# Kernel optimization log

Measured on AMD Instinct MI355X. Metric: run time of the kernel, lower is better.

The kernel has to match this reference:

```python
import jax, jax.numpy as jnp
import numpy as np
from jax import lax

IN_CH = 512
OUT_CH = 512
HEAD_DIM = 8
NUM_HEADS = IN_CH // HEAD_DIM  # 64
INNER = NUM_HEADS * HEAD_DIM   # 512
KSIZE = 5
EPS = 1e-15
BN_EPS = 1e-5
DN = ('NCHW', 'OIHW', 'NCHW')


def setup_inputs() -> dict:
    key = jax.random.key(0)
    ks = jax.random.split(key, 10)
    s = 0.02
    return {
        'hidden_states': jax.random.normal(ks[0], (4, IN_CH, 64, 64), jnp.float32),
        'wq': jax.random.normal(ks[1], (INNER, IN_CH), jnp.float32) * s,
        'wk': jax.random.normal(ks[2], (INNER, IN_CH), jnp.float32) * s,
        'wv': jax.random.normal(ks[3], (INNER, IN_CH), jnp.float32) * s,
        # depthwise conv: groups = 3*INNER, 1 in-channel per group
        'dw_kernel': jax.random.normal(ks[4], (3 * INNER, 1, KSIZE, KSIZE), jnp.float32) * s,
        # grouped 1x1 conv: groups = 3*NUM_HEADS -> 3*INNER/(3*NUM_HEADS)=HEAD_DIM in-ch/group
        'pw_kernel': jax.random.normal(ks[5], (3 * INNER, HEAD_DIM, 1, 1), jnp.float32) * s,
        # proj_out 1x1: in = INNER*(1+len(kernel_sizes)) = 2*INNER
        'proj_kernel': jax.random.normal(ks[6], (OUT_CH, 2 * INNER, 1, 1), jnp.float32) * s,
        'bn_gamma': jnp.ones((OUT_CH,), jnp.float32),
        'bn_beta': jnp.zeros((OUT_CH,), jnp.float32),
        'bn_mean': jnp.zeros((OUT_CH,), jnp.float32),
        'bn_var': jnp.ones((OUT_CH,), jnp.float32),
    }


def _forward(hidden_states, wq, wk, wv, dw_kernel, pw_kernel, proj_kernel,
             bn_gamma, bn_beta, bn_mean, bn_var):
    x = hidden_states  # [B,C,H,W]
    B, _, H, W = x.shape
    h = jnp.moveaxis(x, 1, -1)  # [B,H,W,C]
    q = h @ wq.T
    k = h @ wk.T
    v = h @ wv.T
    qkv = jnp.moveaxis(jnp.concatenate([q, k, v], axis=-1), -1, 1)  # [B,3*INNER,H,W]

    # multi-scale aggregation: depthwise 5x5 then grouped 1x1
    dw = lax.conv_general_dilated(qkv, dw_kernel, (1, 1), 'SAME',
                                  feature_group_count=3 * INNER, dimension_numbers=DN)
    pw = lax.conv_general_dilated(dw, pw_kernel, (1, 1), 'VALID',
                                  feature_group_count=3 * NUM_HEADS, dimension_numbers=DN)
    qkv_all = jnp.concatenate([qkv, pw], axis=1)  # [B, 2*3*INNER, H, W]

    # relu linear attention (fp32)
    N = H * W
    d = HEAD_DIM
    f = qkv_all.astype(jnp.float32).reshape(B, -1, 3 * d, N)  # [B, nh_total, 3d, N]
    query = jax.nn.relu(f[:, :, :d])
    key_ = jax.nn.relu(f[:, :, d:2 * d])
    value = f[:, :, 2 * d:]
    value_pad = jnp.concatenate([value, jnp.ones_like(value[:, :, :1])], axis=2)  # [B,nh,d+1,N]
    scores = jnp.einsum('bhdn,bhen->bhde', value_pad, key_)   # [B,nh,d+1,d]
    out = jnp.einsum('bhde,bhen->bhdn', scores, query)         # [B,nh,d+1,N]
    out = out[:, :, :-1] / (out[:, :, -1:] + EPS)
    out = out.reshape(B, -1, H, W).astype(qkv_all.dtype)        # [B, 2*INNER, H, W]

    # proj_out 1x1 conv + BatchNorm2d (eval mode, running stats)
    y = lax.conv_general_dilated(out, proj_kernel, (1, 1), 'VALID', dimension_numbers=DN)
    inv = bn_gamma / jnp.sqrt(bn_var + BN_EPS)
    y = y * inv[None, :, None, None] + (bn_beta - bn_mean * inv)[None, :, None, None]
    return y + x


def reference(hidden_states, wq, wk, wv, dw_kernel, pw_kernel, proj_kernel,
              bn_gamma, bn_beta, bn_mean, bn_var):
    return _forward(hidden_states, wq, wk, wv, dw_kernel, pw_kernel, proj_kernel,
                    bn_gamma, bn_beta, bn_mean, bn_var)
```

## Files before the change

### kernel.cpp

```cpp
#include <hip/hip_runtime.h>
#include <hip/hip_bf16.h>

typedef __hip_bfloat16 bf16;
typedef __attribute__((ext_vector_type(8))) short bf16x8;
typedef __attribute__((ext_vector_type(4))) float f32x4;

#define BATCH 4
#define CIN   512
#define HW    64
#define NPIX  4096
#define CALL  3072
#define NHEAD 128
#define EPS_LITE 1e-15f
#define BN_EPS   1e-5f


__device__ __forceinline__ short f2bf(float f) {
    __hip_bfloat16 h = __float2bfloat16(f);
    short s; __builtin_memcpy(&s, &h, 2); return s;
}
__device__ __forceinline__ float bfl(unsigned u) {
    unsigned v = u << 16; float f; __builtin_memcpy(&f, &v, 4); return f;
}
__device__ __forceinline__ float bfh(unsigned u) {
    unsigned v = u & 0xffff0000u; float f; __builtin_memcpy(&f, &v, 4); return f;
}
__device__ __forceinline__ unsigned packbf(float a, float b) {
    return (unsigned)(unsigned short)f2bf(a) | ((unsigned)(unsigned short)f2bf(b) << 16);
}
__device__ __forceinline__ void gll16(const void* gsrc, void* ldst) {
    __builtin_amdgcn_global_load_lds(
        (const __attribute__((address_space(1))) unsigned int*)gsrc,
        (__attribute__((address_space(3))) unsigned int*)ldst, 16, 0, 0);
}

__global__ __launch_bounds__(256) void k_cvtw(const float* __restrict__ wq,
                                              const float* __restrict__ wk,
                                              const float* __restrict__ wv,
                                              const float* __restrict__ pj,
                                              bf16* __restrict__ Wbf,
                                              bf16* __restrict__ Pbf) {
    const int e = (blockIdx.x * 256 + threadIdx.x) * 4;
    const float* s; bf16* dst;
    if (e < 786432) {
        int o;
        if (e < 262144)      { s = wq; o = e; }
        else if (e < 524288) { s = wk; o = e - 262144; }
        else                 { s = wv; o = e - 524288; }
        f32x4 v = *(const f32x4*)(s + o);
        dst = Wbf + e;
        *(ushort2*)dst = make_ushort2((unsigned short)f2bf(v[0]), (unsigned short)f2bf(v[1]));
        *(ushort2*)(dst + 2) = make_ushort2((unsigned short)f2bf(v[2]), (unsigned short)f2bf(v[3]));
    } else {
        const int o = e - 786432;
        f32x4 v = *(const f32x4*)(pj + o);
        dst = Pbf + o;
        *(ushort2*)dst = make_ushort2((unsigned short)f2bf(v[0]), (unsigned short)f2bf(v[1]));
        *(ushort2*)(dst + 2) = make_ushort2((unsigned short)f2bf(v[2]), (unsigned short)f2bf(v[3]));
    }
}

__global__ __launch_bounds__(256) void k_cvtx(const float* __restrict__ x,
                                              bf16* __restrict__ xT) {
    __shared__ short lds[64][72];
    const int t   = threadIdx.x;
    const int px0 = blockIdx.x * 64;
    const int k0  = blockIdx.y * 64;
    const int b   = blockIdx.z;

    const int pr = t & 15, rr = t >> 4;
#pragma unroll
    for (int it = 0; it < 4; ++it) {
        const int row = it * 16 + rr;
        f32x4 v = *(const f32x4*)(x + (size_t)(b * CIN + k0 + row) * NPIX + px0 + pr * 4);
#pragma unroll
        for (int i = 0; i < 4; ++i) lds[pr * 4 + i][row] = f2bf(v[i]);
    }
    __syncthreads();

    const int px = t >> 2, kc = t & 3;
    uint4 u0 = *(const uint4*)&lds[px][kc * 16];
    uint4 u1 = *(const uint4*)&lds[px][kc * 16 + 8];
    bf16* dst = xT + ((size_t)b * NPIX + px0 + px) * 512 + k0 + kc * 16;
    *(uint4*)dst = u0;
    *(uint4*)(dst + 8) = u1;
}

template<int KD, int MT, bool PROJ>
__global__ __launch_bounds__(256) void k_gemm3(
        const bf16* __restrict__ Xt,
        const bf16* __restrict__ Wb,
        bf16* __restrict__ Obf,
        const float* __restrict__ gm, const float* __restrict__ bt,
        const float* __restrict__ mu, const float* __restrict__ va,
        const float* __restrict__ resid, float* __restrict__ Of)
{
    constexpr int NT = KD / 32;
    constexpr int MS = MT / 32;
    constexpr int AG = MT / 64;
    __shared__ short Ald[2][MT * 32];
    __shared__ short Bld[2][128 * 32];

    const int t    = threadIdx.x;
    const int lane = t & 63;
    const int w    = t >> 6;
    const int wm   = w >> 1, wn = w & 1;
    const int n0   = blockIdx.x * 128;
    const int c0   = blockIdx.y * MT;
    const int b    = blockIdx.z;

    const bf16* abase = Wb + (size_t)(c0 + w * (MT / 4) + (lane >> 2)) * KD + (lane & 3) * 8;
    const bf16* bbase = Xt + ((size_t)b * NPIX + n0 + w * 32 + (lane >> 2)) * KD + (lane & 3) * 8;

    auto stage = [&](int s, int buf) {
#pragma unroll
        for (int q = 0; q < AG; ++q)
            gll16(abase + (size_t)q * 16 * KD + s * 32,
                  &Ald[buf][(w * (MT / 4) + q * 16) * 32]);
#pragma unroll
        for (int q = 0; q < 2; ++q)
            gll16(bbase + (size_t)q * 16 * KD + s * 32,
                  &Bld[buf][(w * 32 + q * 16) * 32]);
    };

    f32x4 acc[MS][4];
#pragma unroll
    for (int ms = 0; ms < MS; ++ms)
#pragma unroll
        for (int ns = 0; ns < 4; ++ns)
#pragma unroll
            for (int j = 0; j < 4; ++j) acc[ms][ns][j] = 0.f;

    stage(0, 0);
    __syncthreads();

    const int l15 = lane & 15, l4 = lane >> 4;
    for (int s = 0; s < NT; ++s) {
        const int cur = s & 1;
        if (s + 1 < NT) stage(s + 1, cur ^ 1);

        bf16x8 af[MS], bv[4];
#pragma unroll
        for (int ms = 0; ms < MS; ++ms)
            af[ms] = *(const bf16x8*)&Ald[cur][(wm * (MT / 2) + ms * 16 + l15) * 32 + l4 * 8];
#pragma unroll
        for (int ns = 0; ns < 4; ++ns)
            bv[ns] = *(const bf16x8*)&Bld[cur][(wn * 64 + ns * 16 + l15) * 32 + l4 * 8];
#pragma unroll
        for (int ms = 0; ms < MS; ++ms)
#pragma unroll
            for (int ns = 0; ns < 4; ++ns)
                acc[ms][ns] = __builtin_amdgcn_mfma_f32_16x16x32_bf16(
                    af[ms], bv[ns], acc[ms][ns], 0, 0, 0);

        __syncthreads();
    }

    if (!PROJ) {
#pragma unroll
        for (int ms = 0; ms < MS; ++ms) {
            const int crow = c0 + wm * (MT / 2) + ms * 16 + l4 * 4;
#pragma unroll
            for (int ns = 0; ns < 4; ++ns) {
                const int ncol = n0 + wn * 64 + ns * 16 + l15;
#pragma unroll
                for (int j = 0; j < 4; ++j) {
                    bf16 h; short sv = f2bf(acc[ms][ns][j]);
                    __builtin_memcpy(&h, &sv, 2);
                    Obf[((size_t)b * CALL + crow + j) * NPIX + ncol] = h;
                }
            }
        }
    } else {
#pragma unroll
        for (int ms = 0; ms < MS; ++ms) {
            const int crow = c0 + wm * (MT / 2) + ms * 16 + l4 * 4;
#pragma unroll
            for (int j = 0; j < 4; ++j) {
                const int o = crow + j;
                const float inv = gm[o] / sqrtf(va[o] + BN_EPS);
                const float sh  = bt[o] - mu[o] * inv;
#pragma unroll
                for (int ns = 0; ns < 4; ++ns) {
                    const int ncol = n0 + wn * 64 + ns * 16 + l15;
                    const size_t idx = ((size_t)b * 512 + o) * NPIX + ncol;
                    Of[idx] = acc[ms][ns][j] * inv + sh + resid[idx];
                }
            }
        }
    }
}

#define DW_ICS 1608
#define DW_DCS 1032
__global__ __launch_bounds__(256) void k_dwpw(const float* __restrict__ dwk,
                                              const float* __restrict__ pwk,
                                              bf16* __restrict__ qkv_all) {
    __shared__ short slds[8 * DW_ICS];

    const int t  = threadIdx.x;
    const int g  = blockIdx.y;
    const int b  = blockIdx.z;
    const int y0 = blockIdx.x * 16;

    const bf16* src = qkv_all + ((size_t)b * CALL + g * 8) * NPIX;
#pragma unroll
    for (int i = 0; i < 7; ++i) {
        const int v = i * 256 + t;
        if (v < 1600) {
            const int ch  = v / 200;
            const int rem = v % 200;
            const int row = rem / 10;
            const int seg = rem % 10;
            const int grow = y0 + row - 2;
            uint4 val = make_uint4(0u, 0u, 0u, 0u);
            if (seg >= 1 && seg <= 8 && grow >= 0 && grow < HW)
                val = *(const uint4*)(src + (size_t)ch * NPIX + grow * HW + (seg - 1) * 8);
            *(uint4*)&slds[ch * DW_ICS + row * 80 + seg * 8] = val;
        }
    }

    const int lane = t & 63;
    const int w    = t >> 6;
    const int xb   = lane & 7;
    const int ch   = lane >> 3;
    const int x0   = xb * 8;

    float kc[25];
    {
        const float* kp = dwk + (size_t)(g * 8 + ch) * 25;
#pragma unroll
        for (int i = 0; i < 25; ++i) kc[i] = kp[i];
    }
    __syncthreads();

    float A[5][12];
    const short* cb = &slds[ch * DW_ICS + x0];

    auto loadrow = [&](int L, float* f) {
        const short* rp = cb + L * 80;
        uint2 lo = *(const uint2*)(rp + 4);
        uint4 md = *(const uint4*)(rp + 8);
        uint2 hi = *(const uint2*)(rp + 16);
        f[0]  = bfl(lo.y); f[1]  = bfh(lo.y);
        f[2]  = bfl(md.x); f[3]  = bfh(md.x);
        f[4]  = bfl(md.y); f[5]  = bfh(md.y);
        f[6]  = bfl(md.z); f[7]  = bfh(md.z);
        f[8]  = bfl(md.w); f[9]  = bfh(md.w);
        f[10] = bfl(hi.x); f[11] = bfh(hi.x);
    };

    const int r0 = w * 4;
    loadrow(r0 + 0, A[0]);
    loadrow(r0 + 1, A[1]);
    loadrow(r0 + 2, A[2]);
    loadrow(r0 + 3, A[3]);

    uint4 pk[4];
#pragma unroll
    for (int ri = 0; ri < 4; ++ri) {
        loadrow(r0 + ri + 4, A[(ri + 4) % 5]);
        float acc[8];
#pragma unroll
        for (int i = 0; i < 8; ++i) acc[i] = 0.f;
#pragma unroll
        for (int dy = 0; dy < 5; ++dy) {
            const float* Ar = A[(ri + dy) % 5];
#pragma unroll
            for (int dx = 0; dx < 5; ++dx) {
                const float kv = kc[dy * 5 + dx];
#pragma unroll
                for (int i = 0; i < 8; ++i)
                    acc[i] += Ar[i + dx] * kv;
            }
        }
        pk[ri].x = packbf(acc[0], acc[1]);
        pk[ri].y = packbf(acc[2], acc[3]);
        pk[ri].z = packbf(acc[4], acc[5]);
        pk[ri].w = packbf(acc[6], acc[7]);
    }
    __syncthreads();

#pragma unroll
    for (int ri = 0; ri < 4; ++ri)
        *(uint4*)&slds[ch * DW_DCS + (r0 + ri) * 64 + x0] = pk[ri];
    __syncthreads();

    const float* pwb = pwk + (size_t)g * 64;
#pragma unroll
    for (int it = 0; it < 2; ++it) {
        const int p2 = (it * 256 + t) * 2;
        float v0[8], v1[8];
#pragma unroll
        for (int ci = 0; ci < 8; ++ci) {
            const unsigned u = *(const unsigned*)&slds[ci * DW_DCS + p2];
            v0[ci] = bfl(u); v1[ci] = bfh(u);
        }
        bf16* op = qkv_all + ((size_t)b * CALL + 1536 + g * 8) * NPIX + y0 * HW + p2;
#pragma unroll
        for (int o = 0; o < 8; ++o) {
            float s0 = 0.f, s1 = 0.f;
#pragma unroll
            for (int ci = 0; ci < 8; ++ci) {
                const float wv = pwb[o * 8 + ci];
                s0 += wv * v0[ci]; s1 += wv * v1[ci];
            }
            *(unsigned*)(op + (size_t)o * NPIX) = packbf(s0, s1);
        }
    }
}

__global__ __launch_bounds__(64) void k_scores(const bf16* __restrict__ qkv_all,
                                               float* __restrict__ part) {
    const int lane = threadIdx.x;
    const int h = blockIdx.y;
    const int b = blockIdx.z;
    const bf16* base = qkv_all + ((size_t)b * CALL + h * 24) * NPIX;

    float acc[72];
#pragma unroll
    for (int i = 0; i < 72; ++i) acc[i] = 0.f;

    for (int it = 0; it < 4; ++it) {
        const int n = blockIdx.x * 512 + it * 128 + lane * 2;
        const bf16* p = base + n;
        float k0[8], k1[8], v0[8], v1[8];
#pragma unroll
        for (int e = 0; e < 8; ++e) {
            const unsigned u = *(const unsigned*)&p[(size_t)(8 + e) * NPIX];
            k0[e] = fmaxf(bfl(u), 0.f); k1[e] = fmaxf(bfh(u), 0.f);
        }
#pragma unroll
        for (int d = 0; d < 8; ++d) {
            const unsigned u = *(const unsigned*)&p[(size_t)(16 + d) * NPIX];
            v0[d] = bfl(u); v1[d] = bfh(u);
        }
#pragma unroll
        for (int d = 0; d < 9; ++d) {
            const float vd0 = (d < 8) ? v0[d] : 1.f;
            const float vd1 = (d < 8) ? v1[d] : 1.f;
#pragma unroll
            for (int e = 0; e < 8; ++e)
                acc[d * 8 + e] += vd0 * k0[e] + vd1 * k1[e];
        }
    }

    const int bh = b * NHEAD + h;
#pragma unroll
    for (int i = 0; i < 72; ++i) {
        float v = acc[i];
        for (int off = 32; off; off >>= 1) v += __shfl_xor(v, off, 64);
        if (lane == 0) part[((size_t)bh * 72 + i) * 8 + blockIdx.x] = v;
    }
}

__global__ __launch_bounds__(256) void k_att3(const bf16* __restrict__ qkv_all,
                                              const float* __restrict__ part,
                                              bf16* __restrict__ attT) {
    __shared__ float sc[72];
    const int t  = threadIdx.x;
    const int h  = blockIdx.y;
    const int b  = blockIdx.z;
    const int bh = b * NHEAD + h;

    if (t < 72) {
        float s = 0.f;
#pragma unroll
        for (int ns = 0; ns < 8; ++ns) s += part[((size_t)bh * 72 + t) * 8 + ns];
        sc[t] = s;
    }
    __syncthreads();

    const int px = blockIdx.x * 256 + t;
    const bf16* qb = qkv_all + ((size_t)b * CALL + h * 24) * NPIX + px;
    float q[8];
#pragma unroll
    for (int e = 0; e < 8; ++e)
        q[e] = fmaxf(__bfloat162float(qb[(size_t)e * NPIX]), 0.f);

    float num[9];
#pragma unroll
    for (int d = 0; d < 9; ++d) {
        float s = 0.f;
#pragma unroll
        for (int e = 0; e < 8; ++e) s += sc[d * 8 + e] * q[e];
        num[d] = s;
    }
    const float inv = 1.f / (num[8] + EPS_LITE);
    uint4 pk;
    pk.x = packbf(num[0] * inv, num[1] * inv);
    pk.y = packbf(num[2] * inv, num[3] * inv);
    pk.z = packbf(num[4] * inv, num[5] * inv);
    pk.w = packbf(num[6] * inv, num[7] * inv);
    *(uint4*)(attT + ((size_t)b * NPIX + px) * 1024 + h * 8) = pk;
}

extern "C" void kernel_launch(void* const* d_in, const int* in_sizes, int n_in,
                              void* d_out, int out_size, void* d_ws, size_t ws_size,
                              hipStream_t stream) {
    const float* x   = (const float*)d_in[0];
    const float* wq  = (const float*)d_in[1];
    const float* wk  = (const float*)d_in[2];
    const float* wv  = (const float*)d_in[3];
    const float* dwk = (const float*)d_in[4];
    const float* pwk = (const float*)d_in[5];
    const float* pj  = (const float*)d_in[6];
    const float* gm  = (const float*)d_in[7];
    const float* bt  = (const float*)d_in[8];
    const float* mu  = (const float*)d_in[9];
    const float* va  = (const float*)d_in[10];
    float* out = (float*)d_out;

    char* ws = (char*)d_ws;
    bf16*  qkv_all = (bf16*)(ws);
    bf16*  attT    = (bf16*)(ws + 100663296);
    bf16*  xT      = (bf16*)(ws + 100663296);
    float* part    = (float*)(ws + 134217728);
    bf16*  Wbf     = (bf16*)(ws + 135544832);
    bf16*  Pbf     = (bf16*)(ws + 137117696);

    k_cvtw<<<dim3(1280), 256, 0, stream>>>(wq, wk, wv, pj, Wbf, Pbf);
    k_cvtx<<<dim3(64, 8, BATCH), 256, 0, stream>>>(x, xT);
    k_gemm3<512, 128, false><<<dim3(32, 12, BATCH), 256, 0, stream>>>(
        xT, Wbf, qkv_all, nullptr, nullptr, nullptr, nullptr, nullptr, nullptr);
    k_dwpw  <<<dim3( 4, 192, BATCH), 256, 0, stream>>>(dwk, pwk, qkv_all);
    k_scores<<<dim3( 8, 128, BATCH),  64, 0, stream>>>(qkv_all, part);
    k_att3  <<<dim3(16, 128, BATCH), 256, 0, stream>>>(qkv_all, part, attT);
    k_gemm3<1024, 64, true><<<dim3(32, 8, BATCH), 256, 0, stream>>>(
        attT, Pbf, nullptr, gm, bt, mu, va, x, out);
}
```

Baseline: 172.9 us.

## Merge conversion kernels and co-schedule independent attention stages in shared launches

Merges the weight and input conversion kernels into one launch. The depthwise/pointwise stage now shares a launch with the scores computation for the first 64 heads, which depend only on the GEMM output. A second launch pairs scores for the upper heads with attention output for the lower heads, and the remaining attention runs in a third launch. The aim is fewer launches and better GPU fill by overlapping independent work, at the cost of extra branching and shared-memory sizing set by the largest body.

New measurement: 226.0 us. +30.8%, slower.

```diff
diff --git a/kernel.cpp b/kernel.cpp
--- a/kernel.cpp
+++ b/kernel.cpp
@@ -34,56 +34,59 @@
         (__attribute__((address_space(3))) unsigned int*)ldst, 16, 0, 0);
 }
 
-__global__ __launch_bounds__(256) void k_cvtw(const float* __restrict__ wq,
-                                              const float* __restrict__ wk,
-                                              const float* __restrict__ wv,
-                                              const float* __restrict__ pj,
-                                              bf16* __restrict__ Wbf,
-                                              bf16* __restrict__ Pbf) {
-    const int e = (blockIdx.x * 256 + threadIdx.x) * 4;
-    const float* s; bf16* dst;
-    if (e < 786432) {
-        int o;
-        if (e < 262144)      { s = wq; o = e; }
-        else if (e < 524288) { s = wk; o = e - 262144; }
-        else                 { s = wv; o = e - 524288; }
-        f32x4 v = *(const f32x4*)(s + o);
-        dst = Wbf + e;
-        *(ushort2*)dst = make_ushort2((unsigned short)f2bf(v[0]), (unsigned short)f2bf(v[1]));
-        *(ushort2*)(dst + 2) = make_ushort2((unsigned short)f2bf(v[2]), (unsigned short)f2bf(v[3]));
+__global__ __launch_bounds__(256) void k_cvt(const float* __restrict__ x,
+                                             const float* __restrict__ wq,
+                                             const float* __restrict__ wk,
+                                             const float* __restrict__ wv,
+                                             const float* __restrict__ pj,
+                                             bf16* __restrict__ xT,
+                                             bf16* __restrict__ Wbf,
+                                             bf16* __restrict__ Pbf) {
+    __shared__ short lds[64][72];
+    const int bid = blockIdx.x;
+    const int t   = threadIdx.x;
+
+    if (bid < 2048) {
+        const int px0 = (bid & 63) * 64;
+        const int k0  = ((bid >> 6) & 7) * 64;
+        const int b   = bid >> 9;
+
+        const int pr = t & 15, rr = t >> 4;
+#pragma unroll
+        for (int it = 0; it < 4; ++it) {
+            const int row = it * 16 + rr;
+            f32x4 v = *(const f32x4*)(x + (size_t)(b * CIN + k0 + row) * NPIX + px0 + pr * 4);
+#pragma unroll
+            for (int i = 0; i < 4; ++i) lds[pr * 4 + i][row] = f2bf(v[i]);
+        }
+        __syncthreads();
+
+        const int px = t >> 2, kc = t & 3;
+        uint4 u0 = *(const uint4*)&lds[px][kc * 16];
+        uint4 u1 = *(const uint4*)&lds[px][kc * 16 + 8];
+        bf16* dst = xT + ((size_t)b * NPIX + px0 + px) * 512 + k0 + kc * 16;
+        *(uint4*)dst = u0;
+        *(uint4*)(dst + 8) = u1;
     } else {
-        const int o = e - 786432;
-        f32x4 v = *(const f32x4*)(pj + o);
-        dst = Pbf + o;
-        *(ushort2*)dst = make_ushort2((unsigned short)f2bf(v[0]), (unsigned short)f2bf(v[1]));
-        *(ushort2*)(dst + 2) = make_ushort2((unsigned short)f2bf(v[2]), (unsigned short)f2bf(v[3]));
-    }
-}
-
-__global__ __launch_bounds__(256) void k_cvtx(const float* __restrict__ x,
-                                              bf16* __restrict__ xT) {
-    __shared__ short lds[64][72];
-    const int t   = threadIdx.x;
-    const int px0 = blockIdx.x * 64;
-    const int k0  = blockIdx.y * 64;
-    const int b   = blockIdx.z;
-
-    const int pr = t & 15, rr = t >> 4;
-#pragma unroll
-    for (int it = 0; it < 4; ++it) {
-        const int row = it * 16 + rr;
-        f32x4 v = *(const f32x4*)(x + (size_t)(b * CIN + k0 + row) * NPIX + px0 + pr * 4);
-#pragma unroll
-        for (int i = 0; i < 4; ++i) lds[pr * 4 + i][row] = f2bf(v[i]);
-    }
-    __syncthreads();
-
-    const int px = t >> 2, kc = t & 3;
-    uint4 u0 = *(const uint4*)&lds[px][kc * 16];
-    uint4 u1 = *(const uint4*)&lds[px][kc * 16 + 8];
-    bf16* dst = xT + ((size_t)b * NPIX + px0 + px) * 512 + k0 + kc * 16;
-    *(uint4*)dst = u0;
-    *(uint4*)(dst + 8) = u1;
+        const int e = ((bid - 2048) * 256 + t) * 4;
+        const float* s; bf16* dst;
+        if (e < 786432) {
+            int o;
+            if (e < 262144)      { s = wq; o = e; }
+            else if (e < 524288) { s = wk; o = e - 262144; }
+            else                 { s = wv; o = e - 524288; }
+            f32x4 v = *(const f32x4*)(s + o);
+            dst = Wbf + e;
+            *(ushort2*)dst = make_ushort2((unsigned short)f2bf(v[0]), (unsigned short)f2bf(v[1]));
+            *(ushort2*)(dst + 2) = make_ushort2((unsigned short)f2bf(v[2]), (unsigned short)f2bf(v[3]));
+        } else {
+            const int o = e - 786432;
+            f32x4 v = *(const f32x4*)(pj + o);
+            dst = Pbf + o;
+            *(ushort2*)dst = make_ushort2((unsigned short)f2bf(v[0]), (unsigned short)f2bf(v[1]));
+            *(ushort2*)(dst + 2) = make_ushort2((unsigned short)f2bf(v[2]), (unsigned short)f2bf(v[3]));
+        }
+    }
 }
 
 template<int KD, int MT, bool PROJ>
@@ -193,15 +196,14 @@
 
 #define DW_ICS 1608
 #define DW_DCS 1032
-__global__ __launch_bounds__(256) void k_dwpw(const float* __restrict__ dwk,
-                                              const float* __restrict__ pwk,
-                                              bf16* __restrict__ qkv_all) {
-    __shared__ short slds[8 * DW_ICS];
-
+
+__device__ __forceinline__ void dwpw_body(const float* __restrict__ dwk,
+                                          const float* __restrict__ pwk,
+                                          bf16* __restrict__ qkv_all,
+                                          short* slds,
+                                          int ytile, int g, int b) {
     const int t  = threadIdx.x;
-    const int g  = blockIdx.y;
-    const int b  = blockIdx.z;
-    const int y0 = blockIdx.x * 16;
+    const int y0 = ytile * 16;
 
     const bf16* src = qkv_all + ((size_t)b * CALL + g * 8) * NPIX;
 #pragma unroll
@@ -310,11 +312,10 @@
     }
 }
 
-__global__ __launch_bounds__(64) void k_scores(const bf16* __restrict__ qkv_all,
-                                               float* __restrict__ part) {
-    const int lane = threadIdx.x;
-    const int h = blockIdx.y;
-    const int b = blockIdx.z;
+__device__ __forceinline__ void scores_body(const bf16* __restrict__ qkv_all,
+                                            float* __restrict__ part,
+                                            int ns, int h, int b) {
+    const int lane = threadIdx.x & 63;
     const bf16* base = qkv_all + ((size_t)b * CALL + h * 24) * NPIX;
 
     float acc[72];
@@ -322,7 +323,7 @@
     for (int i = 0; i < 72; ++i) acc[i] = 0.f;
 
     for (int it = 0; it < 4; ++it) {
-        const int n = blockIdx.x * 512 + it * 128 + lane * 2;
+        const int n = ns * 512 + it * 128 + lane * 2;
         const bf16* p = base + n;
         float k0[8], k1[8], v0[8], v1[8];
 #pragma unroll
@@ -350,28 +351,27 @@
     for (int i = 0; i < 72; ++i) {
         float v = acc[i];
         for (int off = 32; off; off >>= 1) v += __shfl_xor(v, off, 64);
-        if (lane == 0) part[((size_t)bh * 72 + i) * 8 + blockIdx.x] = v;
-    }
-}
-
-__global__ __launch_bounds__(256) void k_att3(const bf16* __restrict__ qkv_all,
-                                              const float* __restrict__ part,
-                                              bf16* __restrict__ attT) {
-    __shared__ float sc[72];
+        if (lane == 0) part[((size_t)bh * 72 + i) * 8 + ns] = v;
+    }
+}
+
+__device__ __forceinline__ void att_body(const bf16* __restrict__ qkv_all,
+                                         const float* __restrict__ part,
+                                         bf16* __restrict__ attT,
+                                         float* sc,
+                                         int xt, int h, int b) {
     const int t  = threadIdx.x;
-    const int h  = blockIdx.y;
-    const int b  = blockIdx.z;
     const int bh = b * NHEAD + h;
 
     if (t < 72) {
         float s = 0.f;
 #pragma unroll
-        for (int ns = 0; ns < 8; ++ns) s += part[((size_t)bh * 72 + t) * 8 + ns];
+        for (int nss = 0; nss < 8; ++nss) s += part[((size_t)bh * 72 + t) * 8 + nss];
         sc[t] = s;
     }
     __syncthreads();
 
-    const int px = blockIdx.x * 256 + t;
+    const int px = xt * 256 + t;
     const bf16* qb = qkv_all + ((size_t)b * CALL + h * 24) * NPIX + px;
     float q[8];
 #pragma unroll
@@ -393,6 +393,46 @@
     pk.z = packbf(num[4] * inv, num[5] * inv);
     pk.w = packbf(num[6] * inv, num[7] * inv);
     *(uint4*)(attT + ((size_t)b * NPIX + px) * 1024 + h * 8) = pk;
+}
+
+__global__ __launch_bounds__(256, 4) void k_fuse1(const float* __restrict__ dwk,
+                                                  const float* __restrict__ pwk,
+                                                  bf16* __restrict__ qkv_all,
+                                                  float* __restrict__ part) {
+    __shared__ short slds[8 * DW_ICS];
+    const int bid = blockIdx.x;
+    if (bid < 512) {
+        const int ns = bid & 7, hg = (bid >> 3) & 15, b = bid >> 7;
+        const int h  = hg * 4 + (threadIdx.x >> 6);
+        scores_body(qkv_all, part, ns, h, b);
+    } else {
+        const int db = bid - 512;
+        const int ytile = db & 3, g = (db >> 2) % 192, b = db / 768;
+        dwpw_body(dwk, pwk, qkv_all, slds, ytile, g, b);
+    }
+}
+
+__global__ __launch_bounds__(256, 4) void k_fuse2(const bf16* __restrict__ qkv_all,
+                                                  float* __restrict__ part,
+                                                  bf16* __restrict__ attT) {
+    __shared__ float sc[72];
+    const int bid = blockIdx.x;
+    if (bid < 512) {
+        const int ns = bid & 7, hg = (bid >> 3) & 15, b = bid >> 7;
+        const int h  = 64 + hg * 4 + (threadIdx.x >> 6);
+        scores_body(qkv_all, part, ns, h, b);
+    } else {
+        const int ab = bid - 512;
+        const int xt = ab & 15, h = (ab >> 4) & 63, b = ab >> 10;
+        att_body(qkv_all, part, attT, sc, xt, h, b);
+    }
+}
+
+__global__ __launch_bounds__(256) void k_att_hi(const bf16* __restrict__ qkv_all,
+                                                const float* __restrict__ part,
+                                                bf16* __restrict__ attT) {
+    __shared__ float sc[72];
+    att_body(qkv_all, part, attT, sc, blockIdx.x, blockIdx.y + 64, blockIdx.z);
 }
 
 extern "C" void kernel_launch(void* const* d_in, const int* in_sizes, int n_in,
@@ -419,13 +459,12 @@
     bf16*  Wbf     = (bf16*)(ws + 135544832);
     bf16*  Pbf     = (bf16*)(ws + 137117696);
 
-    k_cvtw<<<dim3(1280), 256, 0, stream>>>(wq, wk, wv, pj, Wbf, Pbf);
-    k_cvtx<<<dim3(64, 8, BATCH), 256, 0, stream>>>(x, xT);
+    k_cvt<<<dim3(3328), 256, 0, stream>>>(x, wq, wk, wv, pj, xT, Wbf, Pbf);
     k_gemm3<512, 128, false><<<dim3(32, 12, BATCH), 256, 0, stream>>>(
         xT, Wbf, qkv_all, nullptr, nullptr, nullptr, nullptr, nullptr, nullptr);
-    k_dwpw  <<<dim3( 4, 192, BATCH), 256, 0, stream>>>(dwk, pwk, qkv_all);
-    k_scores<<<dim3( 8, 128, BATCH),  64, 0, stream>>>(qkv_all, part);
-    k_att3  <<<dim3(16, 128, BATCH), 256, 0, stream>>>(qkv_all, part, attT);
+    k_fuse1 <<<dim3(3584), 256, 0, stream>>>(dwk, pwk, qkv_all, part);
+    k_fuse2 <<<dim3(4608), 256, 0, stream>>>(qkv_all, part, attT);
+    k_att_hi<<<dim3(16, 64, BATCH), 256, 0, stream>>>(qkv_all, part, attT);
     k_gemm3<1024, 64, true><<<dim3(32, 8, BATCH), 256, 0, stream>>>(
         attT, Pbf, nullptr, gm, bt, mu, va, x, out);
 }
```

## Merge conversion kernels and double-buffer row tiles in depthwise/pointwise kernel

Applied to the files above, without the earlier changes.

The weight and input conversion kernels are combined into one launch that picks its role from the block index, removing one kernel launch. The depthwise+pointwise kernel now handles two 16-row tiles per block and prefetches the second tile's global loads into registers while the first tile is computed, to hide load latency. The pointwise accumulation is written as 2-wide float vector operations. In exchange it uses more registers, which may lower occupancy, and launches half as many dwpw blocks.

Result: faster. 166.8 us (-3.5%).

```diff
diff --git a/kernel.cpp b/kernel.cpp
--- a/kernel.cpp
+++ b/kernel.cpp
@@ -4,6 +4,7 @@
 typedef __hip_bfloat16 bf16;
 typedef __attribute__((ext_vector_type(8))) short bf16x8;
 typedef __attribute__((ext_vector_type(4))) float f32x4;
+typedef __attribute__((ext_vector_type(2))) float f32v2;
 
 #define BATCH 4
 #define CIN   512
@@ -34,56 +35,59 @@
         (__attribute__((address_space(3))) unsigned int*)ldst, 16, 0, 0);
 }
 
-__global__ __launch_bounds__(256) void k_cvtw(const float* __restrict__ wq,
-                                              const float* __restrict__ wk,
-                                              const float* __restrict__ wv,
-                                              const float* __restrict__ pj,
-                                              bf16* __restrict__ Wbf,
-                                              bf16* __restrict__ Pbf) {
-    const int e = (blockIdx.x * 256 + threadIdx.x) * 4;
-    const float* s; bf16* dst;
-    if (e < 786432) {
-        int o;
-        if (e < 262144)      { s = wq; o = e; }
-        else if (e < 524288) { s = wk; o = e - 262144; }
-        else                 { s = wv; o = e - 524288; }
-        f32x4 v = *(const f32x4*)(s + o);
-        dst = Wbf + e;
-        *(ushort2*)dst = make_ushort2((unsigned short)f2bf(v[0]), (unsigned short)f2bf(v[1]));
-        *(ushort2*)(dst + 2) = make_ushort2((unsigned short)f2bf(v[2]), (unsigned short)f2bf(v[3]));
+__global__ __launch_bounds__(256) void k_cvt(const float* __restrict__ x,
+                                             const float* __restrict__ wq,
+                                             const float* __restrict__ wk,
+                                             const float* __restrict__ wv,
+                                             const float* __restrict__ pj,
+                                             bf16* __restrict__ xT,
+                                             bf16* __restrict__ Wbf,
+                                             bf16* __restrict__ Pbf) {
+    __shared__ short lds[64][72];
+    const int bid = blockIdx.x;
+    const int t   = threadIdx.x;
+
+    if (bid < 2048) {
+        const int px0 = (bid & 63) * 64;
+        const int k0  = ((bid >> 6) & 7) * 64;
+        const int b   = bid >> 9;
+
+        const int pr = t & 15, rr = t >> 4;
+#pragma unroll
+        for (int it = 0; it < 4; ++it) {
+            const int row = it * 16 + rr;
+            f32x4 v = *(const f32x4*)(x + (size_t)(b * CIN + k0 + row) * NPIX + px0 + pr * 4);
+#pragma unroll
+            for (int i = 0; i < 4; ++i) lds[pr * 4 + i][row] = f2bf(v[i]);
+        }
+        __syncthreads();
+
+        const int px = t >> 2, kc = t & 3;
+        uint4 u0 = *(const uint4*)&lds[px][kc * 16];
+        uint4 u1 = *(const uint4*)&lds[px][kc * 16 + 8];
+        bf16* dst = xT + ((size_t)b * NPIX + px0 + px) * 512 + k0 + kc * 16;
+        *(uint4*)dst = u0;
+        *(uint4*)(dst + 8) = u1;
     } else {
-        const int o = e - 786432;
-        f32x4 v = *(const f32x4*)(pj + o);
-        dst = Pbf + o;
-        *(ushort2*)dst = make_ushort2((unsigned short)f2bf(v[0]), (unsigned short)f2bf(v[1]));
-        *(ushort2*)(dst + 2) = make_ushort2((unsigned short)f2bf(v[2]), (unsigned short)f2bf(v[3]));
-    }
-}
-
-__global__ __launch_bounds__(256) void k_cvtx(const float* __restrict__ x,
-                                              bf16* __restrict__ xT) {
-    __shared__ short lds[64][72];
-    const int t   = threadIdx.x;
-    const int px0 = blockIdx.x * 64;
-    const int k0  = blockIdx.y * 64;
-    const int b   = blockIdx.z;
-
-    const int pr = t & 15, rr = t >> 4;
-#pragma unroll
-    for (int it = 0; it < 4; ++it) {
-        const int row = it * 16 + rr;
-        f32x4 v = *(const f32x4*)(x + (size_t)(b * CIN + k0 + row) * NPIX + px0 + pr * 4);
-#pragma unroll
-        for (int i = 0; i < 4; ++i) lds[pr * 4 + i][row] = f2bf(v[i]);
-    }
-    __syncthreads();
-
-    const int px = t >> 2, kc = t & 3;
-    uint4 u0 = *(const uint4*)&lds[px][kc * 16];
-    uint4 u1 = *(const uint4*)&lds[px][kc * 16 + 8];
-    bf16* dst = xT + ((size_t)b * NPIX + px0 + px) * 512 + k0 + kc * 16;
-    *(uint4*)dst = u0;
-    *(uint4*)(dst + 8) = u1;
+        const int e = ((bid - 2048) * 256 + t) * 4;
+        const float* s; bf16* dst;
+        if (e < 786432) {
+            int o;
+            if (e < 262144)      { s = wq; o = e; }
+            else if (e < 524288) { s = wk; o = e - 262144; }
+            else                 { s = wv; o = e - 524288; }
+            f32x4 v = *(const f32x4*)(s + o);
+            dst = Wbf + e;
+            *(ushort2*)dst = make_ushort2((unsigned short)f2bf(v[0]), (unsigned short)f2bf(v[1]));
+            *(ushort2*)(dst + 2) = make_ushort2((unsigned short)f2bf(v[2]), (unsigned short)f2bf(v[3]));
+        } else {
+            const int o = e - 786432;
+            f32x4 v = *(const f32x4*)(pj + o);
+            dst = Pbf + o;
+            *(ushort2*)dst = make_ushort2((unsigned short)f2bf(v[0]), (unsigned short)f2bf(v[1]));
+            *(ushort2*)(dst + 2) = make_ushort2((unsigned short)f2bf(v[2]), (unsigned short)f2bf(v[3]));
+        }
+    }
 }
 
 template<int KD, int MT, bool PROJ>
@@ -198,27 +202,12 @@
                                               bf16* __restrict__ qkv_all) {
     __shared__ short slds[8 * DW_ICS];
 
-    const int t  = threadIdx.x;
-    const int g  = blockIdx.y;
-    const int b  = blockIdx.z;
-    const int y0 = blockIdx.x * 16;
+    const int t   = threadIdx.x;
+    const int g   = blockIdx.y;
+    const int b   = blockIdx.z;
+    const int yt0 = blockIdx.x * 2;
 
     const bf16* src = qkv_all + ((size_t)b * CALL + g * 8) * NPIX;
-#pragma unroll
-    for (int i = 0; i < 7; ++i) {
-        const int v = i * 256 + t;
-        if (v < 1600) {
-            const int ch  = v / 200;
-            const int rem = v % 200;
-            const int row = rem / 10;
-            const int seg = rem % 10;
-            const int grow = y0 + row - 2;
-            uint4 val = make_uint4(0u, 0u, 0u, 0u);
-            if (seg >= 1 && seg <= 8 && grow >= 0 && grow < HW)
-                val = *(const uint4*)(src + (size_t)ch * NPIX + grow * HW + (seg - 1) * 8);
-            *(uint4*)&slds[ch * DW_ICS + row * 80 + seg * 8] = val;
-        }
-    }
 
     const int lane = t & 63;
     const int w    = t >> 6;
@@ -226,88 +215,132 @@
     const int ch   = lane >> 3;
     const int x0   = xb * 8;
 
+    const int sv   = t;
+    auto tload = [&](int ytile, uint4* r) {
+        const int y0 = ytile * 16;
+#pragma unroll
+        for (int i = 0; i < 7; ++i) {
+            const int v = i * 256 + sv;
+            uint4 val = make_uint4(0u, 0u, 0u, 0u);
+            if (v < 1600) {
+                const int c  = v / 200;
+                const int rm = v % 200;
+                const int rw = rm / 10;
+                const int sg = rm % 10;
+                const int grow = y0 + rw - 2;
+                if (sg >= 1 && sg <= 8 && grow >= 0 && grow < HW)
+                    val = *(const uint4*)(src + (size_t)c * NPIX + grow * HW + (sg - 1) * 8);
+            }
+            r[i] = val;
+        }
+    };
+    auto twrite = [&](const uint4* r) {
+#pragma unroll
+        for (int i = 0; i < 7; ++i) {
+            const int v = i * 256 + sv;
+            if (v < 1600) {
+                const int c  = v / 200;
+                const int rm = v % 200;
+                const int rw = rm / 10;
+                const int sg = rm % 10;
+                *(uint4*)&slds[c * DW_ICS + rw * 80 + sg * 8] = r[i];
+            }
+        }
+    };
+
     float kc[25];
     {
         const float* kp = dwk + (size_t)(g * 8 + ch) * 25;
 #pragma unroll
         for (int i = 0; i < 25; ++i) kc[i] = kp[i];
     }
+
+    auto compute_tile = [&](int ytile) {
+        const int y0 = ytile * 16;
+        float A[5][12];
+        const short* cb = &slds[ch * DW_ICS + x0];
+
+        auto loadrow = [&](int L, float* f) {
+            const short* rp = cb + L * 80;
+            uint2 lo = *(const uint2*)(rp + 4);
+            uint4 md = *(const uint4*)(rp + 8);
+            uint2 hi = *(const uint2*)(rp + 16);
+            f[0]  = bfl(lo.y); f[1]  = bfh(lo.y);
+            f[2]  = bfl(md.x); f[3]  = bfh(md.x);
+            f[4]  = bfl(md.y); f[5]  = bfh(md.y);
+            f[6]  = bfl(md.z); f[7]  = bfh(md.z);
+            f[8]  = bfl(md.w); f[9]  = bfh(md.w);
+            f[10] = bfl(hi.x); f[11] = bfh(hi.x);
+        };
+
+        const int rr0 = w * 4;
+        loadrow(rr0 + 0, A[0]);
+        loadrow(rr0 + 1, A[1]);
+        loadrow(rr0 + 2, A[2]);
+        loadrow(rr0 + 3, A[3]);
+
+        uint4 pk[4];
+#pragma unroll
+        for (int ri = 0; ri < 4; ++ri) {
+            loadrow(rr0 + ri + 4, A[(ri + 4) % 5]);
+            float acc[8];
+#pragma unroll
+            for (int i = 0; i < 8; ++i) acc[i] = 0.f;
+#pragma unroll
+            for (int dy = 0; dy < 5; ++dy) {
+                const float* Ar = A[(ri + dy) % 5];
+#pragma unroll
+                for (int dx = 0; dx < 5; ++dx) {
+                    const float kv = kc[dy * 5 + dx];
+#pragma unroll
+                    for (int i = 0; i < 8; ++i)
+                        acc[i] += Ar[i + dx] * kv;
+                }
+            }
+            pk[ri].x = packbf(acc[0], acc[1]);
+            pk[ri].y = packbf(acc[2], acc[3]);
+            pk[ri].z = packbf(acc[4], acc[5]);
+            pk[ri].w = packbf(acc[6], acc[7]);
+        }
+        __syncthreads();
+
+#pragma unroll
+        for (int ri = 0; ri < 4; ++ri)
+            *(uint4*)&slds[ch * DW_DCS + (rr0 + ri) * 64 + x0] = pk[ri];
+        __syncthreads();
+
+        const float* pwb = pwk + (size_t)g * 64;
+#pragma unroll
+        for (int it2 = 0; it2 < 2; ++it2) {
+            const int p2 = (it2 * 256 + t) * 2;
+            f32v2 v2[8];
+#pragma unroll
+            for (int ci = 0; ci < 8; ++ci) {
+                const unsigned u = *(const unsigned*)&slds[ci * DW_DCS + p2];
+                v2[ci][0] = bfl(u); v2[ci][1] = bfh(u);
+            }
+            bf16* op = qkv_all + ((size_t)b * CALL + 1536 + g * 8) * NPIX + y0 * HW + p2;
+#pragma unroll
+            for (int o = 0; o < 8; ++o) {
+                f32v2 s2 = {0.f, 0.f};
+#pragma unroll
+                for (int ci = 0; ci < 8; ++ci)
+                    s2 += pwb[o * 8 + ci] * v2[ci];
+                *(unsigned*)(op + (size_t)o * NPIX) = packbf(s2[0], s2[1]);
+            }
+        }
+    };
+
+    uint4 rA[7], rB[7];
+    tload(yt0, rA);
+    twrite(rA);
     __syncthreads();
-
-    float A[5][12];
-    const short* cb = &slds[ch * DW_ICS + x0];
-
-    auto loadrow = [&](int L, float* f) {
-        const short* rp = cb + L * 80;
-        uint2 lo = *(const uint2*)(rp + 4);
-        uint4 md = *(const uint4*)(rp + 8);
-        uint2 hi = *(const uint2*)(rp + 16);
-        f[0]  = bfl(lo.y); f[1]  = bfh(lo.y);
-        f[2]  = bfl(md.x); f[3]  = bfh(md.x);
-        f[4]  = bfl(md.y); f[5]  = bfh(md.y);
-        f[6]  = bfl(md.z); f[7]  = bfh(md.z);
-        f[8]  = bfl(md.w); f[9]  = bfh(md.w);
-        f[10] = bfl(hi.x); f[11] = bfh(hi.x);
-    };
-
-    const int r0 = w * 4;
-    loadrow(r0 + 0, A[0]);
-    loadrow(r0 + 1, A[1]);
-    loadrow(r0 + 2, A[2]);
-    loadrow(r0 + 3, A[3]);
-
-    uint4 pk[4];
-#pragma unroll
-    for (int ri = 0; ri < 4; ++ri) {
-        loadrow(r0 + ri + 4, A[(ri + 4) % 5]);
-        float acc[8];
-#pragma unroll
-        for (int i = 0; i < 8; ++i) acc[i] = 0.f;
-#pragma unroll
-        for (int dy = 0; dy < 5; ++dy) {
-            const float* Ar = A[(ri + dy) % 5];
-#pragma unroll
-            for (int dx = 0; dx < 5; ++dx) {
-                const float kv = kc[dy * 5 + dx];
-#pragma unroll
-                for (int i = 0; i < 8; ++i)
-                    acc[i] += Ar[i + dx] * kv;
-            }
-        }
-        pk[ri].x = packbf(acc[0], acc[1]);
-        pk[ri].y = packbf(acc[2], acc[3]);
-        pk[ri].z = packbf(acc[4], acc[5]);
-        pk[ri].w = packbf(acc[6], acc[7]);
-    }
+    tload(yt0 + 1, rB);
+    compute_tile(yt0);
     __syncthreads();
-
-#pragma unroll
-    for (int ri = 0; ri < 4; ++ri)
-        *(uint4*)&slds[ch * DW_DCS + (r0 + ri) * 64 + x0] = pk[ri];
+    twrite(rB);
     __syncthreads();
-
-    const float* pwb = pwk + (size_t)g * 64;
-#pragma unroll
-    for (int it = 0; it < 2; ++it) {
-        const int p2 = (it * 256 + t) * 2;
-        float v0[8], v1[8];
-#pragma unroll
-        for (int ci = 0; ci < 8; ++ci) {
-            const unsigned u = *(const unsigned*)&slds[ci * DW_DCS + p2];
-            v0[ci] = bfl(u); v1[ci] = bfh(u);
-        }
-        bf16* op = qkv_all + ((size_t)b * CALL + 1536 + g * 8) * NPIX + y0 * HW + p2;
-#pragma unroll
-        for (int o = 0; o < 8; ++o) {
-            float s0 = 0.f, s1 = 0.f;
-#pragma unroll
-            for (int ci = 0; ci < 8; ++ci) {
-                const float wv = pwb[o * 8 + ci];
-                s0 += wv * v0[ci]; s1 += wv * v1[ci];
-            }
-            *(unsigned*)(op + (size_t)o * NPIX) = packbf(s0, s1);
-        }
-    }
+    compute_tile(yt0 + 1);
 }
 
 __global__ __launch_bounds__(64) void k_scores(const bf16* __restrict__ qkv_all,
@@ -419,11 +452,10 @@
     bf16*  Wbf     = (bf16*)(ws + 135544832);
     bf16*  Pbf     = (bf16*)(ws + 137117696);
 
-    k_cvtw<<<dim3(1280), 256, 0, stream>>>(wq, wk, wv, pj, Wbf, Pbf);
-    k_cvtx<<<dim3(64, 8, BATCH), 256, 0, stream>>>(x, xT);
+    k_cvt<<<dim3(3328), 256, 0, stream>>>(x, wq, wk, wv, pj, xT, Wbf, Pbf);
     k_gemm3<512, 128, false><<<dim3(32, 12, BATCH), 256, 0, stream>>>(
         xT, Wbf, qkv_all, nullptr, nullptr, nullptr, nullptr, nullptr, nullptr);
-    k_dwpw  <<<dim3( 4, 192, BATCH), 256, 0, stream>>>(dwk, pwk, qkv_all);
+    k_dwpw  <<<dim3( 2, 192, BATCH), 256, 0, stream>>>(dwk, pwk, qkv_all);
     k_scores<<<dim3( 8, 128, BATCH),  64, 0, stream>>>(qkv_all, part);
     k_att3  <<<dim3(16, 128, BATCH), 256, 0, stream>>>(qkv_all, part, attT);
     k_gemm3<1024, 64, true><<<dim3(32, 8, BATCH), 256, 0, stream>>>(
```
